# Kernel tuning notes

Measured on AMD Instinct MI355X. Metric: run time of the kernel, lower is better.

The kernel has to match this reference:

```python
import jax, jax.numpy as jnp
import numpy as np
from jax import lax

BN_EPS = 1e-5
B, C_IN, HW = 512, 3, 128  # crop batch, channels, crop size
C1, C2 = 32, 64
DIST_THRESHOLD = 0.55


def setup_inputs() -> dict:
    key = jax.random.key(0)
    ks = jax.random.split(key, 13)
    return {
        "crops": jax.random.normal(ks[0], (B, C_IN, HW, HW), jnp.float32),
        "w1": jax.random.normal(ks[1], (C1, C_IN, 3, 3), jnp.float32) * 0.1,
        "b1": jax.random.normal(ks[2], (C1,), jnp.float32) * 0.1,
        "g1": jax.random.uniform(ks[3], (C1,), jnp.float32),
        "be1": jax.random.normal(ks[4], (C1,), jnp.float32) * 0.1,
        "m1": jax.random.normal(ks[5], (C1,), jnp.float32) * 0.1,
        "v1": jax.random.uniform(ks[6], (C1,), jnp.float32),
        "w2": jax.random.normal(ks[7], (C2, C1, 3, 3), jnp.float32) * 0.05,
        "b2": jax.random.normal(ks[8], (C2,), jnp.float32) * 0.1,
        "g2": jax.random.uniform(ks[9], (C2,), jnp.float32),
        "be2": jax.random.normal(ks[10], (C2,), jnp.float32) * 0.1,
        "m2": jax.random.normal(ks[11], (C2,), jnp.float32) * 0.1,
        "v2": jax.random.uniform(ks[12], (C2,), jnp.float32),
    }


def _conv(x, w, b, stride):
    y = lax.conv_general_dilated(
        x, w, window_strides=(stride, stride), padding=((1, 1), (1, 1)),
        dimension_numbers=("NCHW", "OIHW", "NCHW"))
    return y + b[None, :, None, None]


def _bn(x, gamma, beta, mean, var):
    inv = gamma * lax.rsqrt(var + BN_EPS)
    return x * inv[None, :, None, None] + (beta - mean * inv)[None, :, None, None]


def _maxpool2(x):
    return lax.reduce_window(x, -jnp.inf, lax.max, (1, 1, 2, 2), (1, 1, 2, 2), "VALID")


def reference(crops, w1, b1, g1, be1, m1, v1, w2, b2, g2, be2, m2, v2):
    # layer1: Conv(3->32, s1, p1) + BN + ReLU + MaxPool2  -> [B, 32, 64, 64]
    h = _maxpool2(jax.nn.relu(_bn(_conv(crops, w1, b1, 1), g1, be1, m1, v1)))
    # layer2: Conv(32->64, s2, p1) + BN + Sigmoid + MaxPool2 -> [B, 64, 16, 16]
    feat = _maxpool2(jax.nn.sigmoid(_bn(_conv(h, w2, b2, 2), g2, be2, m2, v2)))
    # per-crop distribution score thresholded as in uniqueDistribution/MLE
    scores = feat.mean(axis=(1, 2, 3))            # [B]
    detected = scores >= DIST_THRESHOLD           # [B] bool
    return feat, scores, detected
```

## Files before the change

### kernel.cpp

```cpp
#include <hip/hip_runtime.h>
#include <math.h>

#define BN_EPS 1e-5f
#define HW_ 128

typedef unsigned short u16_t;
typedef unsigned int u32_t;

typedef __bf16 bf16x8 __attribute__((ext_vector_type(8)));
typedef float f32x4 __attribute__((ext_vector_type(4)));
typedef float f32x16 __attribute__((ext_vector_type(16)));
typedef u32_t u32x4 __attribute__((ext_vector_type(4)));
typedef u32_t u32x2 __attribute__((ext_vector_type(2)));
typedef u32x4 u32x4_ma __attribute__((may_alias));
typedef u32x2 u32x2_ma __attribute__((may_alias));

static __device__ __forceinline__ u16_t f2bf(float f) {
    u32_t u = __float_as_uint(f);
    return (u16_t)((u + 0x7FFFu + ((u >> 16) & 1u)) >> 16);
}
static __device__ __forceinline__ u32_t packbf(float a, float b) {
    return (u32_t)f2bf(a) | ((u32_t)f2bf(b) << 16);
}
static __device__ __forceinline__ bf16x8 ld_frag16(const u16_t* p) {
    union { u32x4 u; bf16x8 f; } x;
    x.u = *(const u32x4_ma*)p;
    return x.f;
}
static __device__ __forceinline__ bf16x8 ld_frag32(const u32_t* p) {
    union { u32x4 u; bf16x8 f; } x;
    x.u = *(const u32x4_ma*)p;
    return x.f;
}
static __device__ __forceinline__ bf16x8 asbf(u32x4 u) {
    union { u32x4 u; bf16x8 f; } x;
    x.u = u;
    return x.f;
}

#define WSUM_OFF 0
#define W2R_OFF  512
#define WF_OFF   9728
#define PT_OFF   10496
#define BN1_OFF  13056
#define BN2_OFF  13120
#define WS_TOTAL 13248

#define CI_U32   (36 * 74)

__global__ __launch_bounds__(512) void prep_kernel(
    const float* __restrict__ w1, const float* __restrict__ b1,
    const float* __restrict__ g1, const float* __restrict__ be1,
    const float* __restrict__ m1, const float* __restrict__ v1,
    const float* __restrict__ w2, const float* __restrict__ b2,
    const float* __restrict__ g2, const float* __restrict__ be2,
    const float* __restrict__ m2, const float* __restrict__ v2,
    u32_t* __restrict__ ws)
{
    const int gtid = blockIdx.x * 512 + threadIdx.x;

    if (gtid < 512) ws[WSUM_OFF + gtid] = 0u;

    for (int idx = gtid; idx < 9216; idx += 8192) {
        int H   = idx / 4608;
        int rem = idx - H * 4608;
        int tap = rem >> 9;
        int r2  = rem & 511;
        int ocl = r2 >> 4;
        int icp = r2 & 15;
        const float* wp = w2 + (H * 32 + ocl) * 288 + tap;
        ws[W2R_OFF + idx] = packbf(wp[(2 * icp) * 9], wp[(2 * icp + 1) * 9]);
    }
    if (gtid < 192) {
        int s = gtid >> 6, lane = gtid & 63;
        int n32 = lane & 31, h = lane >> 5;
        u32x4 f;
        #pragma unroll
        for (int jp = 0; jp < 4; ++jp) {
            int j0 = 2 * jp, j1 = 2 * jp + 1;
            int kx0 = 2 * h + (j0 >> 2), ch0 = j0 & 3;
            int kx1 = 2 * h + (j1 >> 2), ch1 = j1 & 3;
            float va = (kx0 < 3 && ch0 < 3) ? w1[n32 * 27 + ch0 * 9 + s * 3 + kx0] : 0.f;
            float vb = (kx1 < 3 && ch1 < 3) ? w1[n32 * 27 + ch1 * 9 + s * 3 + kx1] : 0.f;
            f[jp] = packbf(va, vb);
        }
        ((u32x4_ma*)(ws + WF_OFF))[gtid] = f;
    }
    if (gtid < 2560) {
        int tt = gtid >> 6, lane = gtid & 63;
        int n32 = lane & 31, h = lane >> 5;
        int gA = n32 >> 2, sub = n32 & 3;
        int pA = tt * 8 + gA;
        int gy = (pA * 241) >> 12; gy = min(gy, 16);
        int gx = min(pA - gy * 17, 16); gx = max(gx, 0);
        int cy = 2 * gy + (sub >> 1), cx = 2 * gx + (sub & 1);
        ws[PT_OFF + gtid] = (u32_t)((cy * 37 + cx + 2 * h) * 2);
    }
    if (gtid >= 1024 && gtid < 1056) {
        int ch = gtid - 1024;
        float inv = g1[ch] * rsqrtf(v1[ch] + BN_EPS);
        float sh  = b1[ch] * inv + be1[ch] - m1[ch] * inv;
        ws[BN1_OFF + 2 * ch]     = __float_as_uint(inv);
        ws[BN1_OFF + 2 * ch + 1] = __float_as_uint(sh);
    }
    if (gtid >= 2048 && gtid < 2112) {
        int ch = gtid - 2048;
        float inv = g2[ch] * rsqrtf(v2[ch] + BN_EPS);
        float sh  = b2[ch] * inv + be2[ch] - m2[ch] * inv;
        ws[BN2_OFF + 2 * ch]     = __float_as_uint(inv);
        ws[BN2_OFF + 2 * ch + 1] = __float_as_uint(sh);
    }
}

__global__ __launch_bounds__(512, 8) void fused_cnn_kernel(
    const float* __restrict__ crops, const u32_t* __restrict__ tab,
    float* __restrict__ out, float* __restrict__ wsum)
{
    __shared__ __align__(16) u32_t uniS[CI_U32];
    __shared__ __align__(16) u16_t hS[289 * 32];
    __shared__ float redS[8];

    const int tid  = threadIdx.x;
    const int wave = tid >> 6;
    const int lane = tid & 63;
    const int quad = lane >> 4;
    const int r    = lane & 15;
    const int n32  = lane & 31;
    const int halfk = lane >> 5;

    const int blk = blockIdx.x;
    const int img = blk >> 4;
    const int t   = blk & 15;
    const int fy0 = (t >> 2) * 4;
    const int fx0 = (t & 3) * 4;
    const int crop_y0 = 8 * fy0 - 3;
    const int crop_x0 = 8 * fx0 - 3;
    const bool interior = (fy0 != 0) && (fx0 != 0);

    const float* cbase = crops + (size_t)img * (3 * HW_ * HW_);
    #pragma unroll
    for (int i = 0; i < 3; ++i) {
        int idx = tid + 512 * i;
        if (idx < 1332) {
            int rr = (idx * 1772) >> 16;
            int cc = idx - rr * 37;
            int gr = crop_y0 + rr, gc = crop_x0 + cc;
            float v0 = 0.f, v1v = 0.f, v2v = 0.f;
            if ((unsigned)gr < 128u && (unsigned)gc < 128u) {
                const float* p = cbase + gr * HW_ + gc;
                v0  = p[0];
                v1v = p[HW_ * HW_];
                v2v = p[2 * HW_ * HW_];
            }
            u32x2 w;
            w[0] = packbf(v0, v1v); w[1] = packbf(v2v, 0.f);
            *(u32x2_ma*)&uniS[idx * 2] = w;
        }
    }

    u32x4 wf[3];
    const u32x4_ma* wft = (const u32x4_ma*)(tab + WF_OFF);
    #pragma unroll
    for (int s = 0; s < 3; ++s) wf[s] = wft[s * 64 + lane];
    const float inv1 = __uint_as_float(tab[BN1_OFF + 2 * n32]);
    const float sh1  = __uint_as_float(tab[BN1_OFF + 2 * n32 + 1]);
    __syncthreads();

    const int hsub = n32 & 7;
    const int hchk = n32 >> 3;

    #pragma unroll
    for (int i = 0; i < 5; ++i) {
        int tt = wave + 8 * i;
        const u32_t* bp = uniS + tab[PT_OFF + tt * 64 + lane];

        u32x2 l0a = *(const u32x2_ma*)(bp);
        u32x2 l0b = *(const u32x2_ma*)(bp + 2);
        u32x2 l1a = *(const u32x2_ma*)(bp + 74);
        u32x2 l1b = *(const u32x2_ma*)(bp + 76);
        u32x2 l2a = *(const u32x2_ma*)(bp + 148);
        u32x2 l2b = *(const u32x2_ma*)(bp + 150);
        u32x4 a0; a0[0] = l0a[0]; a0[1] = l0a[1]; a0[2] = l0b[0]; a0[3] = l0b[1];
        u32x4 a1; a1[0] = l1a[0]; a1[1] = l1a[1]; a1[2] = l1b[0]; a1[3] = l1b[1];
        u32x4 a2; a2[0] = l2a[0]; a2[1] = l2a[1]; a2[2] = l2b[0]; a2[3] = l2b[1];

        f32x16 acc = {0.f,0.f,0.f,0.f,0.f,0.f,0.f,0.f,
                      0.f,0.f,0.f,0.f,0.f,0.f,0.f,0.f};
        acc = __builtin_amdgcn_mfma_f32_32x32x16_bf16(asbf(a0), asbf(wf[0]), acc, 0, 0, 0);
        acc = __builtin_amdgcn_mfma_f32_32x32x16_bf16(asbf(a1), asbf(wf[1]), acc, 0, 0, 0);
        acc = __builtin_amdgcn_mfma_f32_32x32x16_bf16(asbf(a2), asbf(wf[2]), acc, 0, 0, 0);

        #pragma unroll
        for (int q = 0; q < 4; ++q) {
            int pD = tt * 8 + 2 * q + halfk;
            float m4 = fmaxf(fmaxf(acc[4 * q], acc[4 * q + 1]),
                             fmaxf(acc[4 * q + 2], acc[4 * q + 3]));
            float val = fmaxf(fmaf(m4, inv1, sh1), 0.f);
            if (!interior) {
                int gyD = (pD * 241) >> 12;
                int gxD = pD - gyD * 17;
                int y2 = 4 * fy0 - 1 + gyD, x2 = 4 * fx0 - 1 + gxD;
                if (y2 < 0 || y2 > 63 || x2 < 0 || x2 > 63) val = 0.f;
            }
            if (pD < 289) {
                int chk = hchk ^ ((pD >> 1) & 3);
                hS[pD * 32 + chk * 8 + hsub] = f2bf(val);
            }
        }
    }
    __syncthreads();

    float* outp = out + (size_t)img * 16384;
    const f32x4 zero4 = {0.f, 0.f, 0.f, 0.f};
    const int mt  = wave & 1;
    const int nt0 = wave >> 1;
    const int cy2 = 2 * nt0 + ((r >> 1) & 1);
    const int cx2 = 2 * (r >> 2) + (r & 1);
    const int fy  = fy0 + nt0;

    const u32_t* wz0 = tab + W2R_OFF + (mt * 16 + r) * 16 + quad * 4;
    const u32_t* wz1 = wz0 + 4608;
    f32x4 acc0 = zero4, acc1 = zero4;
    #pragma unroll
    for (int s = 0; s < 9; ++s) {
        const int ky = s / 3, kx = s - 3 * (s / 3);
        int p = (2 * cy2 + ky) * 17 + (2 * cx2 + kx);
        bf16x8 ah = ld_frag16(&hS[p * 32 + ((quad ^ ((p >> 1) & 3)) << 3)]);
        bf16x8 bw0 = ld_frag32(wz0 + s * 512);
        bf16x8 bw1 = ld_frag32(wz1 + s * 512);
        acc0 = __builtin_amdgcn_mfma_f32_16x16x32_bf16(ah, bw0, acc0, 0, 0, 0);
        acc1 = __builtin_amdgcn_mfma_f32_16x16x32_bf16(ah, bw1, acc1, 0, 0, 0);
    }
    float ssum = 0.f;
    #pragma unroll
    for (int H = 0; H < 2; ++H) {
        f32x4 a = H ? acc1 : acc0;
        const int oc = H * 32 + mt * 16 + r;
        const float s2  = __uint_as_float(tab[BN2_OFF + 2 * oc]);
        const float sh2 = __uint_as_float(tab[BN2_OFF + 2 * oc + 1]);
        float m4 = fmaxf(fmaxf(a[0], a[1]), fmaxf(a[2], a[3]));
        float z = fmaf(m4, s2, sh2);
        float sig = 1.f / (1.f + expf(-z));
        outp[oc * 256 + fy * 16 + fx0 + quad] = sig;
        ssum += sig;
    }

    #pragma unroll
    for (int off = 32; off > 0; off >>= 1)
        ssum += __shfl_xor(ssum, off);
    if (lane == 0) redS[wave] = ssum;
    __syncthreads();
    if (tid == 0) {
        float bs = 0.f;
        #pragma unroll
        for (int w = 0; w < 8; ++w) bs += redS[w];
        atomicAdd(&wsum[img], bs);
    }
}

__global__ void finalize_kernel(const float* __restrict__ ws,
                                float* __restrict__ scores,
                                float* __restrict__ detected) {
    int i = threadIdx.x;
    float mean = ws[i] * (1.f / 16384.f);
    scores[i] = mean;
    detected[i] = (mean >= 0.55f) ? 1.f : 0.f;
}

extern "C" void kernel_launch(void* const* d_in, const int* in_sizes, int n_in,
                              void* d_out, int out_size, void* d_ws, size_t ws_size,
                              hipStream_t stream) {
    (void)in_sizes; (void)n_in; (void)out_size; (void)ws_size;
    const float* crops = (const float*)d_in[0];
    const float* w1  = (const float*)d_in[1];
    const float* b1  = (const float*)d_in[2];
    const float* g1  = (const float*)d_in[3];
    const float* be1 = (const float*)d_in[4];
    const float* m1  = (const float*)d_in[5];
    const float* v1  = (const float*)d_in[6];
    const float* w2  = (const float*)d_in[7];
    const float* b2  = (const float*)d_in[8];
    const float* g2  = (const float*)d_in[9];
    const float* be2 = (const float*)d_in[10];
    const float* m2  = (const float*)d_in[11];
    const float* v2  = (const float*)d_in[12];
    float* out = (float*)d_out;
    u32_t* ws  = (u32_t*)d_ws;

    prep_kernel<<<16, 512, 0, stream>>>(
        w1, b1, g1, be1, m1, v1, w2, b2, g2, be2, m2, v2, ws);
    fused_cnn_kernel<<<8192, 512, 0, stream>>>(
        crops, ws, out, (float*)ws);
    finalize_kernel<<<1, 512, 0, stream>>>(
        (const float*)ws, out + 8388608, out + 8388608 + 512);
}
```

Measured before the change: 273.7 us.

## Vectorize crop loads, prefetch conv2 fragments, use native bf16 cvt and fast exp

Crop staging now loads four consecutive floats per channel as float4 vectors per thread instead of scalar gathers. The bf16 conversion uses the native __bf16 cast so the compiler can emit hardware pack instructions. Patch offsets are loaded into registers and the pool store indices are precomputed. Conv2 software-prefetches the next activation and weight fragments ahead of the MFMAs, and the sigmoid uses __expf. Together these aim to cut global load instruction count and ALU overhead, at the cost of more registers and slightly looser exp accuracy.

After: 266.6 us. 1.03x faster.

```diff
diff --git a/kernel.cpp b/kernel.cpp
--- a/kernel.cpp
+++ b/kernel.cpp
@@ -8,19 +8,27 @@
 typedef unsigned int u32_t;
 
 typedef __bf16 bf16x8 __attribute__((ext_vector_type(8)));
+typedef __bf16 bf16v2 __attribute__((ext_vector_type(2)));
 typedef float f32x4 __attribute__((ext_vector_type(4)));
 typedef float f32x16 __attribute__((ext_vector_type(16)));
 typedef u32_t u32x4 __attribute__((ext_vector_type(4)));
 typedef u32_t u32x2 __attribute__((ext_vector_type(2)));
 typedef u32x4 u32x4_ma __attribute__((may_alias));
 typedef u32x2 u32x2_ma __attribute__((may_alias));
+typedef f32x4 f32x4_ma __attribute__((may_alias));
 
 static __device__ __forceinline__ u16_t f2bf(float f) {
-    u32_t u = __float_as_uint(f);
-    return (u16_t)((u + 0x7FFFu + ((u >> 16) & 1u)) >> 16);
+    union { __bf16 v; u16_t u; } x;
+    x.v = (__bf16)f;
+    return x.u;
 }
 static __device__ __forceinline__ u32_t packbf(float a, float b) {
-    return (u32_t)f2bf(a) | ((u32_t)f2bf(b) << 16);
+    union { bf16v2 v; u32_t u; } x;
+    bf16v2 p;
+    p[0] = (__bf16)a;
+    p[1] = (__bf16)b;
+    x.v = p;
+    return x.u;
 }
 static __device__ __forceinline__ bf16x8 ld_frag16(const u16_t* p) {
     union { u32x4 u; bf16x8 f; } x;
@@ -138,23 +146,41 @@
     const bool interior = (fy0 != 0) && (fx0 != 0);
 
     const float* cbase = crops + (size_t)img * (3 * HW_ * HW_);
-    #pragma unroll
-    for (int i = 0; i < 3; ++i) {
-        int idx = tid + 512 * i;
-        if (idx < 1332) {
-            int rr = (idx * 1772) >> 16;
-            int cc = idx - rr * 37;
-            int gr = crop_y0 + rr, gc = crop_x0 + cc;
-            float v0 = 0.f, v1v = 0.f, v2v = 0.f;
-            if ((unsigned)gr < 128u && (unsigned)gc < 128u) {
-                const float* p = cbase + gr * HW_ + gc;
-                v0  = p[0];
-                v1v = p[HW_ * HW_];
-                v2v = p[2 * HW_ * HW_];
+    const int x0a = crop_x0 - 1;
+    if (tid < 360) {
+        int row = (tid * 6554) >> 16;
+        int vec = tid - row * 10;
+        int gr  = crop_y0 + row;
+        int col0 = x0a + 4 * vec;
+        f32x4 c0 = {0.f,0.f,0.f,0.f}, c1 = {0.f,0.f,0.f,0.f}, c2 = {0.f,0.f,0.f,0.f};
+        if ((unsigned)gr < 128u) {
+            const float* rp = cbase + gr * HW_;
+            if (col0 >= 0 && col0 <= 124) {
+                c0 = *(const f32x4_ma*)(rp + col0);
+                c1 = *(const f32x4_ma*)(rp + HW_ * HW_ + col0);
+                c2 = *(const f32x4_ma*)(rp + 2 * HW_ * HW_ + col0);
+            } else {
+                #pragma unroll
+                for (int j = 0; j < 4; ++j) {
+                    int gc = col0 + j;
+                    if ((unsigned)gc < 128u) {
+                        c0[j] = rp[gc];
+                        c1[j] = rp[HW_ * HW_ + gc];
+                        c2[j] = rp[2 * HW_ * HW_ + gc];
+                    }
+                }
             }
-            u32x2 w;
-            w[0] = packbf(v0, v1v); w[1] = packbf(v2v, 0.f);
-            *(u32x2_ma*)&uniS[idx * 2] = w;
+        }
+        const int ccb = 4 * vec - 1;
+        u32_t* up = uniS + (row * 37 + ccb) * 2;
+        #pragma unroll
+        for (int j = 0; j < 4; ++j) {
+            if ((unsigned)(ccb + j) < 37u) {
+                u32x2 w;
+                w[0] = packbf(c0[j], c1[j]);
+                w[1] = packbf(c2[j], 0.f);
+                *(u32x2_ma*)(up + 2 * j) = w;
+            }
         }
     }
 
@@ -162,18 +188,27 @@
     const u32x4_ma* wft = (const u32x4_ma*)(tab + WF_OFF);
     #pragma unroll
     for (int s = 0; s < 3; ++s) wf[s] = wft[s * 64 + lane];
+    u32_t pofs[5];
+    #pragma unroll
+    for (int i = 0; i < 5; ++i) pofs[i] = tab[PT_OFF + (wave + 8 * i) * 64 + lane];
     const float inv1 = __uint_as_float(tab[BN1_OFF + 2 * n32]);
     const float sh1  = __uint_as_float(tab[BN1_OFF + 2 * n32 + 1]);
     __syncthreads();
 
     const int hsub = n32 & 7;
     const int hchk = n32 >> 3;
-
-    #pragma unroll
-    for (int i = 0; i < 5; ++i) {
-        int tt = wave + 8 * i;
-        const u32_t* bp = uniS + tab[PT_OFF + tt * 64 + lane];
-
+    const int pbase = wave * 8 + halfk;
+
+    int hqi[4];
+    #pragma unroll
+    for (int q = 0; q < 4; ++q)
+        hqi[q] = wave * 256 + halfk * 32 + hsub + q * 64 + ((hchk ^ q) << 3);
+
+    const f32x16 z16 = {0.f,0.f,0.f,0.f,0.f,0.f,0.f,0.f,
+                        0.f,0.f,0.f,0.f,0.f,0.f,0.f,0.f};
+
+    auto conv_trip = [&](int ii) -> f32x16 {
+        const u32_t* bp = uniS + pofs[ii];
         u32x2 l0a = *(const u32x2_ma*)(bp);
         u32x2 l0b = *(const u32x2_ma*)(bp + 2);
         u32x2 l1a = *(const u32x2_ma*)(bp + 74);
@@ -183,30 +218,42 @@
         u32x4 a0; a0[0] = l0a[0]; a0[1] = l0a[1]; a0[2] = l0b[0]; a0[3] = l0b[1];
         u32x4 a1; a1[0] = l1a[0]; a1[1] = l1a[1]; a1[2] = l1b[0]; a1[3] = l1b[1];
         u32x4 a2; a2[0] = l2a[0]; a2[1] = l2a[1]; a2[2] = l2b[0]; a2[3] = l2b[1];
-
-        f32x16 acc = {0.f,0.f,0.f,0.f,0.f,0.f,0.f,0.f,
-                      0.f,0.f,0.f,0.f,0.f,0.f,0.f,0.f};
-        acc = __builtin_amdgcn_mfma_f32_32x32x16_bf16(asbf(a0), asbf(wf[0]), acc, 0, 0, 0);
+        f32x16 acc = __builtin_amdgcn_mfma_f32_32x32x16_bf16(asbf(a0), asbf(wf[0]), z16, 0, 0, 0);
         acc = __builtin_amdgcn_mfma_f32_32x32x16_bf16(asbf(a1), asbf(wf[1]), acc, 0, 0, 0);
         acc = __builtin_amdgcn_mfma_f32_32x32x16_bf16(asbf(a2), asbf(wf[2]), acc, 0, 0, 0);
-
-        #pragma unroll
-        for (int q = 0; q < 4; ++q) {
-            int pD = tt * 8 + 2 * q + halfk;
-            float m4 = fmaxf(fmaxf(acc[4 * q], acc[4 * q + 1]),
-                             fmaxf(acc[4 * q + 2], acc[4 * q + 3]));
-            float val = fmaxf(fmaf(m4, inv1, sh1), 0.f);
-            if (!interior) {
-                int gyD = (pD * 241) >> 12;
-                int gxD = pD - gyD * 17;
-                int y2 = 4 * fy0 - 1 + gyD, x2 = 4 * fx0 - 1 + gxD;
-                if (y2 < 0 || y2 > 63 || x2 < 0 || x2 > 63) val = 0.f;
-            }
-            if (pD < 289) {
-                int chk = hchk ^ ((pD >> 1) & 3);
-                hS[pD * 32 + chk * 8 + hsub] = f2bf(val);
-            }
-        }
+        return acc;
+    };
+
+    auto pool_val = [&](int ii, int q, const f32x16& acc) -> float {
+        float m4 = fmaxf(fmaxf(fmaxf(acc[4 * q], acc[4 * q + 1]), acc[4 * q + 2]),
+                         acc[4 * q + 3]);
+        float val = fmaxf(fmaf(m4, inv1, sh1), 0.f);
+        if (!interior) {
+            int pD  = pbase + ii * 64 + 2 * q;
+            int gyD = (pD * 241) >> 12;
+            int gxD = pD - gyD * 17;
+            int y2 = 4 * fy0 - 1 + gyD, x2 = 4 * fx0 - 1 + gxD;
+            if (y2 < 0 || y2 > 63 || x2 < 0 || x2 > 63) val = 0.f;
+        }
+        return val;
+    };
+
+    #pragma unroll
+    for (int i = 0; i < 4; ++i) {
+        f32x16 acc = conv_trip(i);
+        #pragma unroll
+        for (int q = 0; q < 4; ++q)
+            hS[hqi[q] + i * 2048] = f2bf(pool_val(i, q, acc));
+    }
+    if (wave < 4) {
+        f32x16 acc = conv_trip(4);
+        #pragma unroll
+        for (int q = 0; q < 4; ++q)
+            hS[hqi[q] + 4 * 2048] = f2bf(pool_val(4, q, acc));
+    } else if (wave == 4) {
+        f32x16 acc = conv_trip(4);
+        float val = pool_val(4, 0, acc);
+        if (halfk == 0) hS[hqi[0] + 4 * 2048] = f2bf(val);
     }
     __syncthreads();
 
@@ -217,33 +264,53 @@
     const int cy2 = 2 * nt0 + ((r >> 1) & 1);
     const int cx2 = 2 * (r >> 2) + (r & 1);
     const int fy  = fy0 + nt0;
-
-    const u32_t* wz0 = tab + W2R_OFF + (mt * 16 + r) * 16 + quad * 4;
+    const int p0  = 34 * cy2 + 2 * cx2;
+
+    const int oc0 = mt * 16 + r;
+    const u32_t* wz0 = tab + W2R_OFF + oc0 * 16 + quad * 4;
     const u32_t* wz1 = wz0 + 4608;
+    const float s2_0  = __uint_as_float(tab[BN2_OFF + 2 * oc0]);
+    const float sh2_0 = __uint_as_float(tab[BN2_OFF + 2 * oc0 + 1]);
+    const float s2_1  = __uint_as_float(tab[BN2_OFF + 64 + 2 * oc0]);
+    const float sh2_1 = __uint_as_float(tab[BN2_OFF + 64 + 2 * oc0 + 1]);
+
+    auto ld_ah = [&](int p) -> bf16x8 {
+        return ld_frag16(&hS[p * 32 + (((quad ^ (p >> 1)) & 3) << 3)]);
+    };
+
     f32x4 acc0 = zero4, acc1 = zero4;
+    bf16x8 w0a = ld_frag32(wz0);
+    bf16x8 w1a = ld_frag32(wz1);
+    bf16x8 w0b = ld_frag32(wz0 + 512);
+    bf16x8 w1b = ld_frag32(wz1 + 512);
+    bf16x8 ahn = ld_ah(p0);
     #pragma unroll
     for (int s = 0; s < 9; ++s) {
-        const int ky = s / 3, kx = s - 3 * (s / 3);
-        int p = (2 * cy2 + ky) * 17 + (2 * cx2 + kx);
-        bf16x8 ah = ld_frag16(&hS[p * 32 + ((quad ^ ((p >> 1) & 3)) << 3)]);
-        bf16x8 bw0 = ld_frag32(wz0 + s * 512);
-        bf16x8 bw1 = ld_frag32(wz1 + s * 512);
-        acc0 = __builtin_amdgcn_mfma_f32_16x16x32_bf16(ah, bw0, acc0, 0, 0, 0);
-        acc1 = __builtin_amdgcn_mfma_f32_16x16x32_bf16(ah, bw1, acc1, 0, 0, 0);
-    }
-    float ssum = 0.f;
-    #pragma unroll
-    for (int H = 0; H < 2; ++H) {
-        f32x4 a = H ? acc1 : acc0;
-        const int oc = H * 32 + mt * 16 + r;
-        const float s2  = __uint_as_float(tab[BN2_OFF + 2 * oc]);
-        const float sh2 = __uint_as_float(tab[BN2_OFF + 2 * oc + 1]);
-        float m4 = fmaxf(fmaxf(a[0], a[1]), fmaxf(a[2], a[3]));
-        float z = fmaf(m4, s2, sh2);
-        float sig = 1.f / (1.f + expf(-z));
-        outp[oc * 256 + fy * 16 + fx0 + quad] = sig;
-        ssum += sig;
-    }
+        bf16x8 ah = ahn;
+        if (s < 8) {
+            const int ns = s + 1;
+            const int nky = ns / 3, nkx = ns - 3 * nky;
+            ahn = ld_ah(p0 + nky * 17 + nkx);
+        }
+        bf16x8 cw0 = w0a, cw1 = w1a;
+        w0a = w0b; w1a = w1b;
+        if (s < 7) {
+            w0b = ld_frag32(wz0 + (s + 2) * 512);
+            w1b = ld_frag32(wz1 + (s + 2) * 512);
+        }
+        acc0 = __builtin_amdgcn_mfma_f32_16x16x32_bf16(ah, cw0, acc0, 0, 0, 0);
+        acc1 = __builtin_amdgcn_mfma_f32_16x16x32_bf16(ah, cw1, acc1, 0, 0, 0);
+    }
+
+    float m40 = fmaxf(fmaxf(fmaxf(acc0[0], acc0[1]), acc0[2]), acc0[3]);
+    float z0  = fmaf(m40, s2_0, sh2_0);
+    float sig0 = 1.f / (1.f + __expf(-z0));
+    outp[oc0 * 256 + fy * 16 + fx0 + quad] = sig0;
+    float m41 = fmaxf(fmaxf(fmaxf(acc1[0], acc1[1]), acc1[2]), acc1[3]);
+    float z1  = fmaf(m41, s2_1, sh2_1);
+    float sig1 = 1.f / (1.f + __expf(-z1));
+    outp[(32 + oc0) * 256 + fy * 16 + fx0 + quad] = sig1;
+    float ssum = sig0 + sig1;
 
     #pragma unroll
     for (int off = 32; off > 0; off >>= 1)
```
